# Performance work log

Measured on AMD Instinct MI355X. Metric: run time of the kernel, lower is better.

Reference implementation:

```python
import jax, jax.numpy as jnp
import numpy as np

B, C, N, H = 16, 512, 4096, 512  # batch, visual_channels, visual_flat, hidden_size


def setup_inputs() -> dict:
    key = jax.random.key(0)
    kx, k1, k2, k3, k4 = jax.random.split(key, 5)
    stdv = 1.0 / np.sqrt(H)  # reset_parameters: uniform(-1/sqrt(size(0)), ...), size(0)=H for all weights
    u = lambda k, shape: jax.random.uniform(k, shape, jnp.float32, -stdv, stdv)
    return {
        "visual_inputs": jax.random.normal(kx, (B, C, N), jnp.float32),
        "w_cf": u(k1, (H, N)),  # channel_f: Linear(visual_flat -> hidden)
        "w_cg": u(k2, (H, N)),  # channel_g
        "w_sf": u(k3, (H, C)),  # spatial_f: Conv1d(C -> H, k=1), squeezed
        "w_sg": u(k4, (H, C)),  # spatial_g
    }


def reference(visual_inputs, w_cf, w_cg, w_sf, w_sg):
    x = visual_inputs  # [B, C, N]
    # ---- channel branch: sim[b,c,c'] = <cf[b,c,:], cg[b,c',:]>; summed over dim c then softmax over c'
    cf = jnp.einsum('bcn,hn->bch', x, w_cf)          # [B, C, H]
    cg = jnp.einsum('bcn,hn->bch', x, w_cg)          # [B, C, H]
    # sum_c sim[b,c,c'] = (sum_c cf[b,c,:]) . cg[b,c',:]  -- avoids [B,C,C]
    ch_comp = jnp.einsum('bh,bch->bc', cf.sum(axis=1), cg)        # [B, C]
    channel_mask = jax.nn.softmax(ch_comp, axis=1)[:, :, None]     # [B, C, 1]
    # ---- spatial branch: sim[b,i,j] = <sf[b,:,i], sg[b,:,j]>; summed over dim i then softmax over j
    sf = jnp.einsum('bcn,hc->bhn', x, w_sf)          # [B, H, N]
    sg = jnp.einsum('bcn,hc->bhn', x, w_sg)          # [B, H, N]
    sp_comp = jnp.einsum('bh,bhn->bn', sf.sum(axis=2), sg)         # [B, N]
    spatial_mask = jax.nn.softmax(sp_comp, axis=1)[:, None, :]     # [B, 1, N]
    outputs = x * channel_mask * spatial_mask        # [B, C, N]
    return outputs, channel_mask, spatial_mask
```

## Files before the change

kernel.cpp:

```cpp
#include <hip/hip_runtime.h>

#define Bq 16
#define Cq 512
#define Nq 4096
#define Hq 512

__global__ __launch_bounds__(256) void k1_stats(const float* __restrict__ x,
                                                float* __restrict__ part_xs_n,
                                                float* __restrict__ part_xs_c){
  __shared__ float red[4][256];
  int blk  = blockIdx.x;
  int b    = blk >> 6;
  int nc   = (blk >> 2) & 15;
  int cq   = blk & 3;
  int wave = threadIdx.x >> 6;
  int lane = threadIdx.x & 63;
  int c0   = cq*128 + wave;
  const float* p = x + ((size_t)b*Cq + c0)*Nq + (nc << 8) + (lane << 2);
  float* pc = part_xs_c + ((size_t)(b*16 + nc) << 9) + c0;
  float4 acc = {0.f,0.f,0.f,0.f};
  #pragma unroll 8
  for (int k = 0; k < 32; ++k){
    float4 v = *(const float4*)(p + (size_t)(k*4)*Nq);
    acc.x += v.x; acc.y += v.y; acc.z += v.z; acc.w += v.w;
    float r = (v.x + v.y) + (v.z + v.w);
    #pragma unroll
    for (int off=32; off; off>>=1) r += __shfl_down(r, off, 64);
    if (lane == 0) pc[k*4] = r;
  }
  *(float4*)&red[wave][lane << 2] = acc;
  __syncthreads();
  int t = threadIdx.x;
  part_xs_n[((size_t)(cq*Bq) + b)*Nq + (nc << 8) + t] =
      (red[0][t] + red[1][t]) + (red[2][t] + red[3][t]);
}

__global__ __launch_bounds__(256) void k1b_red(const float* __restrict__ part_xs_n,
                                               const float* __restrict__ part_xs_c,
                                               float* __restrict__ xs_n,
                                               float* __restrict__ xs_c){
  int blk = blockIdx.x;
  if (blk < 256){
    int i = (blk << 8) + (int)threadIdx.x;
    float acc = 0.f;
    #pragma unroll
    for (int cq=0; cq<4; ++cq) acc += part_xs_n[(size_t)cq*(Bq*Nq) + i];
    xs_n[i] = acc;
  } else {
    int j = ((blk-256) << 8) + (int)threadIdx.x;
    int b = j >> 9, c = j & 511;
    float acc = 0.f;
    #pragma unroll
    for (int nc=0; nc<16; ++nc) acc += part_xs_c[((size_t)(b*16+nc) << 9) + c];
    xs_c[j] = acc;
  }
}

__global__ __launch_bounds__(256) void k2_s(const float* __restrict__ w_cf,
                                            const float* __restrict__ w_sf,
                                            const float* __restrict__ xs_n,
                                            const float* __restrict__ xs_c,
                                            float* __restrict__ s_cf,
                                            float* __restrict__ s_sf){
  __shared__ float red[4][Bq];
  int blk = blockIdx.x;
  const float* w; const float* src; float* dst; int L;
  if (blk < Hq) { w = w_cf + (size_t)blk*Nq; src = xs_n; dst = s_cf; L = Nq; }
  else          { w = w_sf + (size_t)(blk-Hq)*Cq; src = xs_c; dst = s_sf; L = Cq; }
  int h = blk & (Hq-1);
  int t = threadIdx.x;
  int wave = t >> 6, lane = t & 63;
  float acc[Bq];
  #pragma unroll
  for (int b=0;b<Bq;b++) acc[b]=0.f;
  for (int i0 = t*4; i0 < L; i0 += 1024){
    float4 wv = *(const float4*)(w + i0);
    #pragma unroll
    for (int b=0;b<Bq;b++){
      float4 sv = *(const float4*)(src + (size_t)b*L + i0);
      acc[b] += wv.x*sv.x + wv.y*sv.y + wv.z*sv.z + wv.w*sv.w;
    }
  }
  #pragma unroll
  for (int b=0;b<Bq;b++){
    float v = acc[b];
    #pragma unroll
    for (int off=32; off; off>>=1) v += __shfl_down(v, off, 64);
    if (lane == 0) red[wave][b] = v;
  }
  __syncthreads();
  if (t < Bq)
    dst[(size_t)t*Hq + h] = (red[0][t]+red[1][t])+(red[2][t]+red[3][t]);
}

__global__ __launch_bounds__(256) void k3_v(const float* __restrict__ w_cg,
                                            const float* __restrict__ w_sg,
                                            const float* __restrict__ s_cf,
                                            const float* __restrict__ s_sf,
                                            float* __restrict__ part_cg,
                                            float* __restrict__ part_sg){
  __shared__ float sl[Bq*64];
  int blk = blockIdx.x;
  const float* w; const float* s; float* dst; int L, jc, hc;
  if (blk < 128){ w=w_cg; s=s_cf; dst=part_cg; L=Nq; jc=blk>>3; hc=blk&7; }
  else { int k=blk-128; w=w_sg; s=s_sf; dst=part_sg; L=Cq; jc=k>>3; hc=k&7; }
  int h0 = hc*64;
  for (int i = threadIdx.x; i < Bq*64; i += 256){
    int b = i >> 6, hh = i & 63;
    sl[i] = s[b*Hq + h0 + hh];
  }
  __syncthreads();
  int j = (jc<<8) + (int)threadIdx.x;
  float acc[Bq];
  #pragma unroll
  for (int b=0;b<Bq;b++) acc[b]=0.f;
  for (int hh=0; hh<64; ++hh){
    float wv = w[(size_t)(h0+hh)*L + j];
    #pragma unroll
    for (int b=0;b<Bq;b++) acc[b] += sl[b*64+hh]*wv;
  }
  #pragma unroll
  for (int b=0;b<Bq;b++) dst[((size_t)hc*Bq + b)*L + j] = acc[b];
}

__global__ __launch_bounds__(256) void k4_comp(const float* __restrict__ x,
                                               const float* __restrict__ part_cg,
                                               const float* __restrict__ part_sg,
                                               float* __restrict__ part_sp,
                                               float* __restrict__ part_ch){
  __shared__ float red[4][256];
  __shared__ float vs[128];
  int blk  = blockIdx.x;
  int b    = blk >> 6;
  int nc   = (blk >> 2) & 15;
  int cq   = blk & 3;
  int wave = threadIdx.x >> 6;
  int lane = threadIdx.x & 63;
  int t    = threadIdx.x;
  if (t < 128){
    int c = cq*128 + t;
    float a = 0.f;
    #pragma unroll
    for (int hc=0; hc<8; ++hc) a += part_sg[((size_t)hc*Bq + b)*Cq + c];
    vs[t] = a;
  }
  int nbase = (nc << 8) + (t << 2) - ((t >> 6) << 8);
  (void)nbase;
  float4 g = {0.f,0.f,0.f,0.f};
  {
    size_t off = (size_t)b*Nq + (nc << 8) + (lane << 2);
    #pragma unroll
    for (int hc=0; hc<8; ++hc){
      float4 pgv = *(const float4*)(part_cg + (size_t)hc*(Bq*Nq) + off);
      g.x += pgv.x; g.y += pgv.y; g.z += pgv.z; g.w += pgv.w;
    }
  }
  __syncthreads();
  int c0 = cq*128 + wave;
  const float* p = x + ((size_t)b*Cq + c0)*Nq + (nc << 8) + (lane << 2);
  float* pc = part_ch + ((size_t)(b*16 + nc) << 9) + c0;
  float4 acc = {0.f,0.f,0.f,0.f};
  #pragma unroll 8
  for (int k = 0; k < 32; ++k){
    float4 v = *(const float4*)(p + (size_t)(k*4)*Nq);
    float s = vs[wave + k*4];
    acc.x += v.x*s; acc.y += v.y*s; acc.z += v.z*s; acc.w += v.w*s;
    float r = v.x*g.x + v.y*g.y + v.z*g.z + v.w*g.w;
    #pragma unroll
    for (int off=32; off; off>>=1) r += __shfl_down(r, off, 64);
    if (lane == 0) pc[k*4] = r;
  }
  *(float4*)&red[wave][lane << 2] = acc;
  __syncthreads();
  part_sp[((size_t)(cq*Bq) + b)*Nq + (nc << 8) + t] =
      (red[0][t] + red[1][t]) + (red[2][t] + red[3][t]);
}

__global__ __launch_bounds__(256) void k5_softmax(const float* __restrict__ part_ch,
                                                  const float* __restrict__ part_sp,
                                                  float* __restrict__ out){
  __shared__ float buf[Nq];
  __shared__ float lds[4];
  __shared__ float bcast;
  int blk = blockIdx.x;
  int t = threadIdx.x;
  float* dst; int L;
  const size_t OUT0 = (size_t)Bq*Cq*Nq;
  if (blk < Bq){
    int b = blk; L = Cq;
    for (int c = t; c < Cq; c += 256){
      float s = 0.f;
      #pragma unroll
      for (int nc=0; nc<16; ++nc) s += part_ch[((size_t)(b*16+nc) << 9) + c];
      buf[c] = s;
    }
    dst = out + OUT0 + (size_t)b*Cq;
  } else {
    int b = blk - Bq; L = Nq;
    for (int n = t; n < Nq; n += 256){
      float s = 0.f;
      #pragma unroll
      for (int cq=0; cq<4; ++cq) s += part_sp[((size_t)(cq*Bq)+b)*Nq + n];
      buf[n] = s;
    }
    dst = out + OUT0 + (size_t)Bq*Cq + (size_t)b*Nq;
  }
  __syncthreads();
  float m = -3.4e38f;
  for (int i=t;i<L;i+=256) m = fmaxf(m, buf[i]);
  #pragma unroll
  for (int off=32; off; off>>=1) m = fmaxf(m, __shfl_down(m, off, 64));
  if ((t&63)==0) lds[t>>6]=m;
  __syncthreads();
  if (t==0) bcast = fmaxf(fmaxf(lds[0],lds[1]),fmaxf(lds[2],lds[3]));
  __syncthreads();
  m = bcast;
  float ssum=0.f;
  for (int i=t;i<L;i+=256) ssum += __expf(buf[i]-m);
  #pragma unroll
  for (int off=32; off; off>>=1) ssum += __shfl_down(ssum, off, 64);
  __syncthreads();
  if ((t&63)==0) lds[t>>6]=ssum;
  __syncthreads();
  if (t==0) bcast = 1.f/((lds[0]+lds[1])+(lds[2]+lds[3]));
  __syncthreads();
  float inv = bcast;
  for (int i=t;i<L;i+=256) dst[i] = __expf(buf[i]-m)*inv;
}

__global__ __launch_bounds__(256) void k6_out(const float* __restrict__ x,
                                              float* __restrict__ out){
  const size_t OUT0 = (size_t)Bq*Cq*Nq;
  const float* cm = out + OUT0;
  const float* sm = out + OUT0 + (size_t)Bq*Cq;
  int blk = blockIdx.x;
  int b = blk >> 11;
  int r = blk & 2047;
  int c = r >> 2;
  int q = r & 3;
  size_t rowoff = ((size_t)b*Cq + c)*Nq;
  int n0 = q*1024 + (int)threadIdx.x*4;
  float4 xv = *(const float4*)(x + rowoff + n0);
  float4 sv = *(const float4*)(sm + (size_t)b*Nq + n0);
  float cmv = cm[b*Cq + c];
  float4 o;
  o.x = xv.x*cmv*sv.x; o.y = xv.y*cmv*sv.y;
  o.z = xv.z*cmv*sv.z; o.w = xv.w*cmv*sv.w;
  *(float4*)(out + rowoff + n0) = o;
}

extern "C" void kernel_launch(void* const* d_in, const int* in_sizes, int n_in,
                              void* d_out, int out_size, void* d_ws, size_t ws_size,
                              hipStream_t stream){
  const float* x    = (const float*)d_in[0];
  const float* w_cf = (const float*)d_in[1];
  const float* w_cg = (const float*)d_in[2];
  const float* w_sf = (const float*)d_in[3];
  const float* w_sg = (const float*)d_in[4];
  float* out = (float*)d_out;

  float* ws = (float*)d_ws;
  float* xs_n = ws;
  float* xs_c = xs_n + Bq*Nq;
  float* s_cf = xs_c + Bq*Cq;
  float* s_sf = s_cf + Bq*Hq;
  float* arenaA = s_sf + Bq*Hq;
  float* part_xs_n = arenaA;
  float* part_xs_c = arenaA + 4*Bq*Nq;
  float* part_cg   = arenaA;
  float* part_sg   = arenaA + 8*Bq*Nq;
  float* arenaB = arenaA + 8*Bq*Nq + 8*Bq*Cq;
  float* part_sp   = arenaB;
  float* part_ch   = arenaB + 4*Bq*Nq;

  k1_stats  <<<1024,    256, 0, stream>>>(x, part_xs_n, part_xs_c);
  k1b_red   <<<288,     256, 0, stream>>>(part_xs_n, part_xs_c, xs_n, xs_c);
  k2_s      <<<2*Hq,    256, 0, stream>>>(w_cf, w_sf, xs_n, xs_c, s_cf, s_sf);
  k3_v      <<<144,     256, 0, stream>>>(w_cg, w_sg, s_cf, s_sf, part_cg, part_sg);
  k4_comp   <<<1024,    256, 0, stream>>>(x, part_cg, part_sg, part_sp, part_ch);
  k5_softmax<<<2*Bq,    256, 0, stream>>>(part_ch, part_sp, out);
  k6_out    <<<Bq*Cq*4, 256, 0, stream>>>(x, out);
}
```

Before: 323.0 us.

## Replace per-row shuffle reductions with LDS staging, split k3 batches, nontemporal output stores

In k1_stats and k4_comp, the per-iteration 64-lane shuffle reductions are replaced. Per-row partials are now staged in LDS and reduced by 128 threads after the barrier, with rotated indexing to avoid bank conflicts. k3_v splits the batch dimension into two halves to double the block count and halve register accumulators. k6_out handles a whole row per block with nontemporal stores to keep the large output from polluting cache. The LDS staging adds about 32KB of shared memory per block, which may reduce occupancy.

```diff
diff --git a/kernel.cpp b/kernel.cpp
--- a/kernel.cpp
+++ b/kernel.cpp
@@ -5,10 +5,13 @@
 #define Nq 4096
 #define Hq 512
 
+typedef float f32x4 __attribute__((ext_vector_type(4)));
+
 __global__ __launch_bounds__(256) void k1_stats(const float* __restrict__ x,
                                                 float* __restrict__ part_xs_n,
                                                 float* __restrict__ part_xs_c){
-  __shared__ float red[4][256];
+  __shared__ float colred[4][256];
+  __shared__ float rowp[4][32][64];
   int blk  = blockIdx.x;
   int b    = blk >> 6;
   int nc   = (blk >> 2) & 15;
@@ -17,22 +20,29 @@
   int lane = threadIdx.x & 63;
   int c0   = cq*128 + wave;
   const float* p = x + ((size_t)b*Cq + c0)*Nq + (nc << 8) + (lane << 2);
-  float* pc = part_xs_c + ((size_t)(b*16 + nc) << 9) + c0;
   float4 acc = {0.f,0.f,0.f,0.f};
   #pragma unroll 8
   for (int k = 0; k < 32; ++k){
     float4 v = *(const float4*)(p + (size_t)(k*4)*Nq);
     acc.x += v.x; acc.y += v.y; acc.z += v.z; acc.w += v.w;
-    float r = (v.x + v.y) + (v.z + v.w);
-    #pragma unroll
-    for (int off=32; off; off>>=1) r += __shfl_down(r, off, 64);
-    if (lane == 0) pc[k*4] = r;
-  }
-  *(float4*)&red[wave][lane << 2] = acc;
+    rowp[wave][k][lane] = (v.x + v.y) + (v.z + v.w);
+  }
+  *(float4*)&colred[wave][lane << 2] = acc;
   __syncthreads();
   int t = threadIdx.x;
   part_xs_n[((size_t)(cq*Bq) + b)*Nq + (nc << 8) + t] =
-      (red[0][t] + red[1][t]) + (red[2][t] + red[3][t]);
+      (colred[0][t] + colred[1][t]) + (colred[2][t] + colred[3][t]);
+  if (t < 128){
+    const float4* rp4 = (const float4*)&rowp[t & 3][t >> 2][0];
+    float4 sv = {0.f,0.f,0.f,0.f};
+    #pragma unroll
+    for (int j4 = 0; j4 < 16; ++j4){
+      float4 vv = rp4[(j4 + t) & 15];
+      sv.x += vv.x; sv.y += vv.y; sv.z += vv.z; sv.w += vv.w;
+    }
+    part_xs_c[((size_t)(b*16 + nc) << 9) + cq*128 + t] =
+        (sv.x + sv.y) + (sv.z + sv.w);
+  }
 }
 
 __global__ __launch_bounds__(256) void k1b_red(const float* __restrict__ part_xs_n,
@@ -99,28 +109,32 @@
                                             const float* __restrict__ s_sf,
                                             float* __restrict__ part_cg,
                                             float* __restrict__ part_sg){
-  __shared__ float sl[Bq*64];
-  int blk = blockIdx.x;
-  const float* w; const float* s; float* dst; int L, jc, hc;
-  if (blk < 128){ w=w_cg; s=s_cf; dst=part_cg; L=Nq; jc=blk>>3; hc=blk&7; }
-  else { int k=blk-128; w=w_sg; s=s_sf; dst=part_sg; L=Cq; jc=k>>3; hc=k&7; }
-  int h0 = hc*64;
-  for (int i = threadIdx.x; i < Bq*64; i += 256){
-    int b = i >> 6, hh = i & 63;
-    sl[i] = s[b*Hq + h0 + hh];
+  __shared__ float sl[8*64];
+  int blk = blockIdx.x;
+  const float* w; const float* s; float* dst; int L, jc, hc, bh;
+  if (blk < 256){ w=w_cg; s=s_cf; dst=part_cg; L=Nq;
+    jc = blk >> 4; hc = (blk >> 1) & 7; bh = blk & 1; }
+  else { int k = blk - 256; w=w_sg; s=s_sf; dst=part_sg; L=Cq;
+    jc = k >> 4; hc = (k >> 1) & 7; bh = k & 1; }
+  int h0 = hc*64, b0 = bh*8;
+  for (int i = threadIdx.x; i < 8*64; i += 256){
+    int bb = i >> 6, hh = i & 63;
+    sl[i] = s[(b0+bb)*Hq + h0 + hh];
   }
   __syncthreads();
   int j = (jc<<8) + (int)threadIdx.x;
-  float acc[Bq];
-  #pragma unroll
-  for (int b=0;b<Bq;b++) acc[b]=0.f;
+  float acc[8];
+  #pragma unroll
+  for (int bb=0;bb<8;bb++) acc[bb]=0.f;
+  #pragma unroll 8
   for (int hh=0; hh<64; ++hh){
     float wv = w[(size_t)(h0+hh)*L + j];
     #pragma unroll
-    for (int b=0;b<Bq;b++) acc[b] += sl[b*64+hh]*wv;
-  }
-  #pragma unroll
-  for (int b=0;b<Bq;b++) dst[((size_t)hc*Bq + b)*L + j] = acc[b];
+    for (int bb=0;bb<8;bb++) acc[bb] += sl[bb*64+hh]*wv;
+  }
+  #pragma unroll
+  for (int bb=0;bb<8;bb++)
+    dst[((size_t)hc*Bq + (b0+bb))*L + j] = acc[bb];
 }
 
 __global__ __launch_bounds__(256) void k4_comp(const float* __restrict__ x,
@@ -128,7 +142,8 @@
                                                const float* __restrict__ part_sg,
                                                float* __restrict__ part_sp,
                                                float* __restrict__ part_ch){
-  __shared__ float red[4][256];
+  __shared__ float colred[4][256];
+  __shared__ float rowp[4][32][64];
   __shared__ float vs[128];
   int blk  = blockIdx.x;
   int b    = blk >> 6;
@@ -144,8 +159,6 @@
     for (int hc=0; hc<8; ++hc) a += part_sg[((size_t)hc*Bq + b)*Cq + c];
     vs[t] = a;
   }
-  int nbase = (nc << 8) + (t << 2) - ((t >> 6) << 8);
-  (void)nbase;
   float4 g = {0.f,0.f,0.f,0.f};
   {
     size_t off = (size_t)b*Nq + (nc << 8) + (lane << 2);
@@ -158,22 +171,29 @@
   __syncthreads();
   int c0 = cq*128 + wave;
   const float* p = x + ((size_t)b*Cq + c0)*Nq + (nc << 8) + (lane << 2);
-  float* pc = part_ch + ((size_t)(b*16 + nc) << 9) + c0;
   float4 acc = {0.f,0.f,0.f,0.f};
   #pragma unroll 8
   for (int k = 0; k < 32; ++k){
     float4 v = *(const float4*)(p + (size_t)(k*4)*Nq);
     float s = vs[wave + k*4];
     acc.x += v.x*s; acc.y += v.y*s; acc.z += v.z*s; acc.w += v.w*s;
-    float r = v.x*g.x + v.y*g.y + v.z*g.z + v.w*g.w;
-    #pragma unroll
-    for (int off=32; off; off>>=1) r += __shfl_down(r, off, 64);
-    if (lane == 0) pc[k*4] = r;
-  }
-  *(float4*)&red[wave][lane << 2] = acc;
+    rowp[wave][k][lane] = v.x*g.x + v.y*g.y + v.z*g.z + v.w*g.w;
+  }
+  *(float4*)&colred[wave][lane << 2] = acc;
   __syncthreads();
   part_sp[((size_t)(cq*Bq) + b)*Nq + (nc << 8) + t] =
-      (red[0][t] + red[1][t]) + (red[2][t] + red[3][t]);
+      (colred[0][t] + colred[1][t]) + (colred[2][t] + colred[3][t]);
+  if (t < 128){
+    const float4* rp4 = (const float4*)&rowp[t & 3][t >> 2][0];
+    float4 sv = {0.f,0.f,0.f,0.f};
+    #pragma unroll
+    for (int j4 = 0; j4 < 16; ++j4){
+      float4 vv = rp4[(j4 + t) & 15];
+      sv.x += vv.x; sv.y += vv.y; sv.z += vv.z; sv.w += vv.w;
+    }
+    part_ch[((size_t)(b*16 + nc) << 9) + cq*128 + t] =
+        (sv.x + sv.y) + (sv.z + sv.w);
+  }
 }
 
 __global__ __launch_bounds__(256) void k5_softmax(const float* __restrict__ part_ch,
@@ -234,19 +254,21 @@
   const float* cm = out + OUT0;
   const float* sm = out + OUT0 + (size_t)Bq*Cq;
   int blk = blockIdx.x;
-  int b = blk >> 11;
-  int r = blk & 2047;
-  int c = r >> 2;
-  int q = r & 3;
-  size_t rowoff = ((size_t)b*Cq + c)*Nq;
-  int n0 = q*1024 + (int)threadIdx.x*4;
-  float4 xv = *(const float4*)(x + rowoff + n0);
-  float4 sv = *(const float4*)(sm + (size_t)b*Nq + n0);
-  float cmv = cm[b*Cq + c];
-  float4 o;
-  o.x = xv.x*cmv*sv.x; o.y = xv.y*cmv*sv.y;
-  o.z = xv.z*cmv*sv.z; o.w = xv.w*cmv*sv.w;
-  *(float4*)(out + rowoff + n0) = o;
+  int b = blk >> 9;
+  size_t rowoff = (size_t)blk * Nq;
+  float cmv = cm[blk];
+  const float* sp = sm + (size_t)b*Nq;
+  int t = threadIdx.x;
+  #pragma unroll
+  for (int q = 0; q < 4; ++q){
+    int n0 = q*1024 + t*4;
+    float4 xv = *(const float4*)(x + rowoff + n0);
+    float4 sv = *(const float4*)(sp + n0);
+    f32x4 o;
+    o.x = xv.x*cmv*sv.x; o.y = xv.y*cmv*sv.y;
+    o.z = xv.z*cmv*sv.z; o.w = xv.w*cmv*sv.w;
+    __builtin_nontemporal_store(o, (f32x4*)(out + rowoff + n0));
+  }
 }
 
 extern "C" void kernel_launch(void* const* d_in, const int* in_sizes, int n_in,
@@ -273,11 +295,11 @@
   float* part_sp   = arenaB;
   float* part_ch   = arenaB + 4*Bq*Nq;
 
-  k1_stats  <<<1024,    256, 0, stream>>>(x, part_xs_n, part_xs_c);
-  k1b_red   <<<288,     256, 0, stream>>>(part_xs_n, part_xs_c, xs_n, xs_c);
-  k2_s      <<<2*Hq,    256, 0, stream>>>(w_cf, w_sf, xs_n, xs_c, s_cf, s_sf);
-  k3_v      <<<144,     256, 0, stream>>>(w_cg, w_sg, s_cf, s_sf, part_cg, part_sg);
-  k4_comp   <<<1024,    256, 0, stream>>>(x, part_cg, part_sg, part_sp, part_ch);
-  k5_softmax<<<2*Bq,    256, 0, stream>>>(part_ch, part_sp, out);
-  k6_out    <<<Bq*Cq*4, 256, 0, stream>>>(x, out);
-}
+  k1_stats  <<<1024,  256, 0, stream>>>(x, part_xs_n, part_xs_c);
+  k1b_red   <<<288,   256, 0, stream>>>(part_xs_n, part_xs_c, xs_n, xs_c);
+  k2_s      <<<2*Hq,  256, 0, stream>>>(w_cf, w_sf, xs_n, xs_c, s_cf, s_sf);
+  k3_v      <<<288,   256, 0, stream>>>(w_cg, w_sg, s_cf, s_sf, part_cg, part_sg);
+  k4_comp   <<<1024,  256, 0, stream>>>(x, part_cg, part_sg, part_sp, part_ch);
+  k5_softmax<<<2*Bq,  256, 0, stream>>>(part_ch, part_sp, out);
+  k6_out    <<<Bq*Cq, 256, 0, stream>>>(x, out);
+}
```

Measured after the change: 328.3 us. No clear change (+1.6%).
